# Kernel optimization log

Measured on AMD Instinct MI355X. Metric: run time of the kernel, lower is better.

## Reference

```python
import jax, jax.numpy as jnp
import numpy as np

HEAD_DIM = 128
NUM_Q_HEAD = 16
NUM_KV_HEAD = 4
WINDOW = 1024
SOFTMAX_CAP = 30.0
SOFTMAX_TEMP = 1.0
CLIP_L, CLIP_R = -0.03, 1.03
SCALE = 1.0 / np.sqrt(HEAD_DIM).astype(np.float32)


def setup_inputs() -> dict:
    key = jax.random.key(0)
    k1, k2, k3 = jax.random.split(key, 3)
    B, S = 2, 2048
    q = jax.random.normal(k1, (B, S, NUM_Q_HEAD, HEAD_DIM), jnp.float32)
    k = jax.random.normal(k2, (B, S, NUM_KV_HEAD, HEAD_DIM), jnp.float32)
    v = jax.random.normal(k3, (B, S, NUM_KV_HEAD, HEAD_DIM), jnp.float32)
    return {"q": q, "k": k, "v": v}


def _sliding_window_attn(q, k, v):
    # q: [B,S,Hq,D]; k,v: [B,S,Hkv,D]  (BSHD layout)
    n_rep = NUM_Q_HEAD // NUM_KV_HEAD
    k = jnp.repeat(k, n_rep, axis=2)  # GQA repeat-interleave -> [B,S,Hq,D]
    v = jnp.repeat(v, n_rep, axis=2)
    # BSHD -> BHSD
    q = q.transpose(0, 2, 1, 3)
    k = k.transpose(0, 2, 1, 3)
    v = v.transpose(0, 2, 1, 3)

    P = jnp.einsum('bhqd,bhkd->bhqk', q, k)  # raw scores [B,H,S,S]

    S = q.shape[2]
    qi = jnp.arange(S)[:, None]
    kj = jnp.arange(S)[None, :]
    # causal + sliding window: allow q_idx - window <= k_idx <= q_idx
    allowed = (kj <= qi) & (kj >= qi - WINDOW)
    mask = jnp.where(allowed, 0.0, -jnp.inf).astype(P.dtype)  # [S,S]

    # softmax capping: cap * tanh(P * scale / temp) + mask
    P = SOFTMAX_CAP * jnp.tanh(P * (SCALE / SOFTMAX_TEMP)) + mask

    A = jax.nn.softmax(P, axis=-1)  # numerically stable (max-subtracted)
    # softmax clipping: clamp((r-l)*A + l, 0, 1); dropout rate is 0 -> identity
    A = jnp.clip((CLIP_R - CLIP_L) * A + CLIP_L, 0.0, 1.0)

    O = jnp.einsum('bhqk,bhkd->bhqd', A, v)
    return O.transpose(0, 2, 1, 3)  # back to BSHD


def reference(q, k, v):
    return _sliding_window_attn(q, k, v)
```

## Files before the change

### kernel.cpp

```cpp
#include <hip/hip_runtime.h>
#include <hip/hip_bf16.h>

typedef float f32x4 __attribute__((ext_vector_type(4)));
typedef _Float16 f16x8 __attribute__((ext_vector_type(8)));
typedef unsigned int u32;

#define SQ   2048
#define HQ   16
#define HKV  4
#define DH   128
#define WIN  1024
#define QT   64
#define KT   64
#define WROW 36

#define AS1 __attribute__((address_space(1)))
#define AS3 __attribute__((address_space(3)))

__device__ __forceinline__ void gload16(const void* g, void* l) {
  __builtin_amdgcn_global_load_lds((const AS1 u32*)g, (AS3 u32*)l, 16, 0, 0);
}

__device__ __forceinline__ float swa_e(float s) {
  float u = __builtin_amdgcn_exp2f(s * 0.25507046054708916f);
  return __builtin_amdgcn_exp2f(-86.5617024533378f * __builtin_amdgcn_rcpf(u + 1.0f));
}

__global__ __launch_bounds__(256)
void prep(const float* __restrict__ K, const float* __restrict__ V,
          _Float16* __restrict__ kf, _Float16* __restrict__ vt)
{
  const int t = blockIdx.x * 256 + threadIdx.x;
  const int NK = 2 * HKV * SQ * 16;
  if (t < NK) {
    const int p  = t & 15;
    const int s  = (t >> 4) & (SQ - 1);
    const int hk = (t >> 15) & 3;
    const int b  = t >> 17;
    const int c  = p ^ (s & 7);
    const float* src = K + (((size_t)b * SQ + s) * HKV + hk) * DH + c * 8;
    f32x4 x0 = *(const f32x4*)src;
    f32x4 x1 = *(const f32x4*)(src + 4);
    f16x8 o;
    #pragma unroll
    for (int j = 0; j < 4; ++j) { o[j] = (_Float16)x0[j]; o[4 + j] = (_Float16)x1[j]; }
    *(f16x8*)(kf + (((size_t)(b * HKV + hk)) * SQ + s) * DH + p * 8) = o;
  } else {
    const int u   = t - NK;
    const int p   = u & 3;
    const int d   = (u >> 2) & 127;
    const int t32 = (u >> 9) & 63;
    const int hk  = (u >> 15) & 3;
    const int b   = u >> 17;
    const int c   = p ^ ((d >> 1) & 3);
    f16x8 o;
    #pragma unroll
    for (int j = 0; j < 8; ++j) {
      const int s = t32 * 32 + c * 8 + j;
      o[j] = (_Float16)V[(((size_t)b * SQ + s) * HKV + hk) * DH + d];
    }
    *(f16x8*)(vt + ((((size_t)(b * HKV + hk)) * 64 + t32) * DH + d) * 32 + p * 8) = o;
  }
}

__global__ __launch_bounds__(256, 4)
void swa_fwd(const float* __restrict__ Q, float* __restrict__ O,
             const _Float16* __restrict__ kf, const _Float16* __restrict__ vt)
{
  __shared__ _Float16 lbuf[16384];
  __shared__ _Float16 lW[4][16 * WROW];

  const int tid  = threadIdx.x;
  const int lane = tid & 63;
  const int wv   = tid >> 6;
  const int lm   = lane & 15;
  const int lg   = lane >> 4;

  const int bid    = blockIdx.x;
  const int stream = bid & 7;
  const int b      = stream >> 2;
  const int hk     = stream & 3;
  const int j      = bid >> 3;
  const int c      = j & 31;
  const int slot   = j >> 5;
  const int i      = c >> 2;
  const int hs     = c & 3;
  const int qt     = (slot == 0) ? (31 - i) : (slot == 1) ? (16 + i)
                   : (slot == 2) ? (15 - i) : i;
  const int h      = hk * 4 + hs;
  const int q0     = qt * QT;

  const _Float16* kfb = kf + ((size_t)(b * HKV + hk)) * SQ * DH;
  const char*     vtb = (const char*)(vt + ((size_t)(b * HKV + hk)) * 64 * DH * 32);

  f16x8 qa[4];
  {
    const int qrow = q0 + wv * 16 + lm;
    const float* qp = Q + (((size_t)b * SQ + qrow) * HQ + h) * DH;
    #pragma unroll
    for (int kb = 0; kb < 4; ++kb) {
      const float* p = qp + kb * 32 + lg * 8;
      f32x4 x0 = *(const f32x4*)p;
      f32x4 x1 = *(const f32x4*)(p + 4);
      f16x8 a;
      #pragma unroll
      for (int jj = 0; jj < 4; ++jj) { a[jj] = (_Float16)x0[jj]; a[4 + jj] = (_Float16)x1[jj]; }
      qa[kb] = a;
    }
  }

  const int kmin = (q0 - WIN) > 0 ? (q0 - WIN) : 0;
  const int nt   = (q0 + QT - kmin) / KT;
  const int qr0  = q0 + wv * 16 + lg * 4;

  #define STAGE16K(dstb, src) do {                                           \
    _Pragma("unroll")                                                        \
    for (int r4 = 0; r4 < 4; ++r4)                                           \
      gload16((const char*)(src) + r4 * 4096 + wv * 1024 + lane * 16,        \
              (char*)lbuf + (dstb) + r4 * 4096 + wv * 1024);                 \
  } while (0)
  #define STAGE8K(dstb, src) do {                                            \
    _Pragma("unroll")                                                        \
    for (int r2 = 0; r2 < 2; ++r2)                                           \
      gload16((const char*)(src) + r2 * 4096 + wv * 1024 + lane * 16,        \
              (char*)lbuf + (dstb) + r2 * 4096 + wv * 1024);                 \
  } while (0)

  float zs[4] = {0.f, 0.f, 0.f, 0.f};
  {
    STAGE16K(0, kfb + (size_t)kmin * DH);
    __syncthreads();
    for (int t = 0; t < nt; ++t) {
      if (t + 1 < nt) STAGE16K(((t + 1) & 1) * 16384, kfb + (size_t)(kmin + (t + 1) * KT) * DH);
      const char* cur  = (const char*)lbuf + (t & 1) * 16384;
      const int  kbase = kmin + t * KT;
      const bool peel  = (t == 0 && q0 >= WIN) || (t == nt - 1);
      #pragma unroll
      for (int ks = 0; ks < 4; ++ks) {
        f32x4 acc = {0.f, 0.f, 0.f, 0.f};
        const int keyl = ks * 16 + lm;
        #pragma unroll
        for (int kb = 0; kb < 4; ++kb) {
          const int chunk = (kb * 4 + lg) ^ (keyl & 7);
          f16x8 bf = *(const f16x8*)(cur + keyl * 256 + chunk * 16);
          acc = __builtin_amdgcn_mfma_f32_16x16x32_f16(qa[kb], bf, acc, 0, 0, 0);
        }
        if (peel) {
          const int key = kbase + keyl;
          #pragma unroll
          for (int r = 0; r < 4; ++r) {
            const int qr = qr0 + r;
            const bool ok = (key <= qr) && (key >= qr - WIN);
            zs[r] += ok ? swa_e(acc[r]) : 0.f;
          }
        } else {
          #pragma unroll
          for (int r = 0; r < 4; ++r) zs[r] += swa_e(acc[r]);
        }
      }
      __syncthreads();
    }
  }

  float rz[4], sthr[4];
  #pragma unroll
  for (int r = 0; r < 4; ++r) {
    float z = zs[r];
    z += __shfl_xor(z, 1);
    z += __shfl_xor(z, 2);
    z += __shfl_xor(z, 4);
    z += __shfl_xor(z, 8);
    rz[r] = 1.06f / z;
    float lt = __log2f(0.0283018868f * z);
    float A  = -86.5617024533378f / lt - 1.0f;
    float sv = 3.9204912f * __log2f(A) - 0.05f;
    sv = (lt >= 0.f) ? 1e30f : sv;
    sv = (lt <= -86.5617f) ? -1e30f : sv;
    sthr[r] = sv;
  }

  f32x4 oacc[8];
  #pragma unroll
  for (int ii = 0; ii < 8; ++ii) oacc[ii] = (f32x4){0.f, 0.f, 0.f, 0.f};

  const int nt2 = (q0 + QT - kmin) >> 5;
  STAGE8K(0,     kfb + (size_t)kmin * DH);
  STAGE8K(16384, vtb + (size_t)(kmin >> 5) * 8192);
  __syncthreads();

  const int vpc = lg ^ ((lm >> 1) & 3);

  for (int t2 = 0; t2 < nt2; ++t2) {
    if (t2 + 1 < nt2) {
      const int kn = kmin + (t2 + 1) * 32;
      STAGE8K(((t2 + 1) & 1) * 8192,         kfb + (size_t)kn * DH);
      STAGE8K(16384 + ((t2 + 1) & 1) * 8192, vtb + (size_t)(kn >> 5) * 8192);
    }
    const char* curK = (const char*)lbuf + (t2 & 1) * 8192;
    const char* curV = (const char*)lbuf + 16384 + (t2 & 1) * 8192;
    const int  kbase = kmin + t2 * 32;
    const bool peel  = ((q0 >= WIN) && (t2 <= 1)) || (t2 >= nt2 - 2);

    #pragma unroll
    for (int ks = 0; ks < 2; ++ks) {
      f32x4 acc = {0.f, 0.f, 0.f, 0.f};
      const int keyl = ks * 16 + lm;
      #pragma unroll
      for (int kb = 0; kb < 4; ++kb) {
        const int chunk = (kb * 4 + lg) ^ (keyl & 7);
        f16x8 bf = *(const f16x8*)(curK + keyl * 256 + chunk * 16);
        acc = __builtin_amdgcn_mfma_f32_16x16x32_f16(qa[kb], bf, acc, 0, 0, 0);
      }
      const int key = kbase + keyl;
      #pragma unroll
      for (int r = 0; r < 4; ++r) {
        float w = 0.f;
        if (__any(acc[r] > sthr[r])) {
          float e = swa_e(acc[r]);
          w = fminf(fmaxf(fmaf(e, rz[r], -0.03f), 0.f), 1.f);
          if (peel) {
            const int qr = qr0 + r;
            const bool ok = (key <= qr) && (key >= qr - WIN);
            w = ok ? w : 0.f;
          }
        }
        lW[wv][(lg * 4 + r) * WROW + ks * 16 + lm] = (_Float16)w;
      }
    }
    const f16x8 af = *(const f16x8*)&lW[wv][lm * WROW + lg * 8];
    #pragma unroll
    for (int dt = 0; dt < 8; ++dt) {
      const int d = dt * 16 + lm;
      f16x8 bf = *(const f16x8*)(curV + d * 64 + vpc * 16);
      oacc[dt] = __builtin_amdgcn_mfma_f32_16x16x32_f16(af, bf, oacc[dt], 0, 0, 0);
    }
    __syncthreads();
  }

  #pragma unroll
  for (int r = 0; r < 4; ++r) {
    float* op = O + (((size_t)b * SQ + (qr0 + r)) * HQ + h) * DH;
    #pragma unroll
    for (int dt = 0; dt < 8; ++dt) op[dt * 16 + lm] = oacc[dt][r];
  }
  #undef STAGE16K
  #undef STAGE8K
}

extern "C" void kernel_launch(void* const* d_in, const int* in_sizes, int n_in,
                              void* d_out, int out_size, void* d_ws, size_t ws_size,
                              hipStream_t stream) {
  const float* q = (const float*)d_in[0];
  const float* k = (const float*)d_in[1];
  const float* v = (const float*)d_in[2];
  float* o = (float*)d_out;

  _Float16* kf = (_Float16*)d_ws;
  _Float16* vt = kf + (size_t)2 * HKV * SQ * DH;

  hipLaunchKernelGGL(prep, dim3(2048), dim3(256), 0, stream, k, v, kf, vt);
  hipLaunchKernelGGL(swa_fwd, dim3(1024), dim3(256), 0, stream, q, o, kf, vt);
}
```

Measured before the change: 87.48 us.

## Prefetch two tiles ahead with partial vmcnt waits instead of full syncthreads

Restructures both the normalizer pass and the weighted-V pass so the next two K/V tiles are in flight at once. Each iteration ends with a plain barrier, then issues the load for tile t+2 into the freed buffer and waits only for the older load with s_waitcnt vmcnt(4). The point is to stop __syncthreads from draining all outstanding global-to-LDS loads, so memory latency overlaps compute more deeply. Scheduling barriers and hand-written waits add fragility: vmcnt counts must match the number of loads issued per stage. A few float constants are also re-rounded.

```diff
diff --git a/kernel.cpp b/kernel.cpp
--- a/kernel.cpp
+++ b/kernel.cpp
@@ -21,9 +21,16 @@
   __builtin_amdgcn_global_load_lds((const AS1 u32*)g, (AS3 u32*)l, 16, 0, 0);
 }
 
+#define BARW(N) do { __builtin_amdgcn_sched_barrier(0);                        \
+  asm volatile("s_waitcnt vmcnt(" #N ")\n\ts_barrier" ::: "memory");           \
+  __builtin_amdgcn_sched_barrier(0); } while (0)
+#define BARP() do { __builtin_amdgcn_sched_barrier(0);                         \
+  asm volatile("s_barrier" ::: "memory");                                      \
+  __builtin_amdgcn_sched_barrier(0); } while (0)
+
 __device__ __forceinline__ float swa_e(float s) {
-  float u = __builtin_amdgcn_exp2f(s * 0.25507046054708916f);
-  return __builtin_amdgcn_exp2f(-86.5617024533378f * __builtin_amdgcn_rcpf(u + 1.0f));
+  float u = __builtin_amdgcn_exp2f(s * 0.2550341464f);
+  return __builtin_amdgcn_exp2f(-86.5617025f * __builtin_amdgcn_rcpf(u + 1.0f));
 }
 
 __global__ __launch_bounds__(256)
@@ -129,9 +136,13 @@
   float zs[4] = {0.f, 0.f, 0.f, 0.f};
   {
     STAGE16K(0, kfb + (size_t)kmin * DH);
-    __syncthreads();
+    if (nt > 1) {
+      STAGE16K(16384, kfb + (size_t)(kmin + KT) * DH);
+      BARW(4);
+    } else {
+      BARW(0);
+    }
     for (int t = 0; t < nt; ++t) {
-      if (t + 1 < nt) STAGE16K(((t + 1) & 1) * 16384, kfb + (size_t)(kmin + (t + 1) * KT) * DH);
       const char* cur  = (const char*)lbuf + (t & 1) * 16384;
       const int  kbase = kmin + t * KT;
       const bool peel  = (t == 0 && q0 >= WIN) || (t == nt - 1);
@@ -158,7 +169,13 @@
           for (int r = 0; r < 4; ++r) zs[r] += swa_e(acc[r]);
         }
       }
-      __syncthreads();
+      BARP();
+      if (t + 2 < nt) {
+        STAGE16K((t & 1) * 16384, kfb + (size_t)(kmin + (t + 2) * KT) * DH);
+        BARW(4);
+      } else {
+        BARW(0);
+      }
     }
   }
 
@@ -172,7 +189,7 @@
     z += __shfl_xor(z, 8);
     rz[r] = 1.06f / z;
     float lt = __log2f(0.0283018868f * z);
-    float A  = -86.5617024533378f / lt - 1.0f;
+    float A  = -86.5617024f / lt - 1.0f;
     float sv = 3.9204912f * __log2f(A) - 0.05f;
     sv = (lt >= 0.f) ? 1e30f : sv;
     sv = (lt <= -86.5617f) ? -1e30f : sv;
@@ -186,16 +203,17 @@
   const int nt2 = (q0 + QT - kmin) >> 5;
   STAGE8K(0,     kfb + (size_t)kmin * DH);
   STAGE8K(16384, vtb + (size_t)(kmin >> 5) * 8192);
-  __syncthreads();
+  if (nt2 > 1) {
+    STAGE8K(8192,         kfb + (size_t)(kmin + 32) * DH);
+    STAGE8K(16384 + 8192, vtb + (size_t)((kmin >> 5) + 1) * 8192);
+    BARW(4);
+  } else {
+    BARW(0);
+  }
 
   const int vpc = lg ^ ((lm >> 1) & 3);
 
   for (int t2 = 0; t2 < nt2; ++t2) {
-    if (t2 + 1 < nt2) {
-      const int kn = kmin + (t2 + 1) * 32;
-      STAGE8K(((t2 + 1) & 1) * 8192,         kfb + (size_t)kn * DH);
-      STAGE8K(16384 + ((t2 + 1) & 1) * 8192, vtb + (size_t)(kn >> 5) * 8192);
-    }
     const char* curK = (const char*)lbuf + (t2 & 1) * 8192;
     const char* curV = (const char*)lbuf + 16384 + (t2 & 1) * 8192;
     const int  kbase = kmin + t2 * 32;
@@ -234,7 +252,15 @@
       f16x8 bf = *(const f16x8*)(curV + d * 64 + vpc * 16);
       oacc[dt] = __builtin_amdgcn_mfma_f32_16x16x32_f16(af, bf, oacc[dt], 0, 0, 0);
     }
-    __syncthreads();
+    BARP();
+    if (t2 + 2 < nt2) {
+      const int kn = kmin + (t2 + 2) * 32;
+      STAGE8K((t2 & 1) * 8192,         kfb + (size_t)kn * DH);
+      STAGE8K(16384 + (t2 & 1) * 8192, vtb + (size_t)(kn >> 5) * 8192);
+      BARW(4);
+    } else {
+      BARW(0);
+    }
   }
 
   #pragma unroll
```

Result: no change. 85.86 us (-1.9%).
